# Kernel tuning notes

Measured on AMD Instinct MI355X. Metric: run time of the kernel, lower is better.

The kernel has to match this reference:

```python
import jax, jax.numpy as jnp
import numpy as np

IN, OUT, STEPS, BATCH = 1024, 1024, 100, 64
THR = 15.0
RATIO = 0.5
C1 = RATIO * THR            # initial membrane potential = 7.5
C2 = 1.0 / THR
C3 = (1.0 - RATIO) / STEPS


def setup_inputs() -> dict:
    key = jax.random.key(0)
    k0, k1, k2, k3 = jax.random.split(key, 4)
    spikes = jax.random.randint(k0, (STEPS, BATCH, IN), 0, 2).astype(jnp.float32)
    mem = jnp.full((BATCH, OUT), C1, dtype=jnp.float32)          # init_if
    hat_spikes = jax.random.uniform(k1, (BATCH, IN), dtype=jnp.float32)
    W = jax.random.normal(k2, (OUT, IN), dtype=jnp.float32)      # w_mean=0, w_std=1
    b = jax.random.normal(k3, (OUT,), dtype=jnp.float32)
    return {"spikes": spikes, "mem": mem, "hat_spikes": hat_spikes, "W": W, "b": b}


def reference(spikes, mem, hat_spikes, W, b):
    steps = spikes.shape[0]
    # delta_us = fc(spikes): [T, B, OUT]
    delta_us = jnp.einsum('tbi,oi->tbo', spikes, W) + b

    def step(carry, du):
        m, su = carry
        m = m + du
        s = (m > THR).astype(m.dtype)          # spike
        m = jnp.clip(m, 0.0, THR)              # clamp_(0, thr)
        su = su + m                            # sum_u += mem
        m = m - m * s                          # reset fired neurons
        return (m, su), s

    (mem_out, sum_u), ss = jax.lax.scan(
        step, (mem, jnp.zeros_like(mem)), delta_us)

    hat_u_fwd = sum_u / steps                  # [B, OUT]
    hat_s_fwd = ss.mean(axis=0)                # [B, OUT]

    # training-mode surrogate path: forward values come from the spike loop,
    # gradients flow through fc(hat_spikes) (ForwardFirstBackwardSecond)
    delta_u = hat_spikes @ W.T + b
    hat_u = jax.lax.stop_gradient(hat_u_fwd) + delta_u - jax.lax.stop_gradient(delta_u)
    surr = jnp.maximum(hat_u * C2, C3)         # (hat_u*C2).clamp_min(C3)
    hat_s = jax.lax.stop_gradient(hat_s_fwd) + surr - jax.lax.stop_gradient(surr)

    return ss, mem_out, hat_s
```

## Files before the change

### kernel.cpp

```cpp
#include <hip/hip_runtime.h>


typedef __attribute__((ext_vector_type(4))) int int4v;

#define T_STEPS 100
#define T_PAD   112
#define BO      65536
#define K_DIM   1024
#define A8_OFF  0
#define BT_OFF  7340032

__global__ __launch_bounds__(256)
void prepass(const float* __restrict__ S, const float* __restrict__ W,
             signed char* __restrict__ A8, signed char* __restrict__ Bt) {
    const int wave = blockIdx.x * 4 + (threadIdx.x >> 6);
    const int lane = threadIdx.x & 63;
    const int r16 = lane & 15, quad = lane >> 4;

    if (wave < 7168) {
        const int b   = wave / 112;
        const int rem = wave - b * 112;
        const int jt  = rem >> 4, k64 = rem & 15;
        const int t   = jt * 16 + r16;
        union { signed char c[16]; int4v v; } u;
        if (t < T_STEPS) {
            const float* sp = S + ((size_t)t * 64 + b) * K_DIM + k64 * 64 + quad * 16;
            const float4 s0 = *(const float4*)(sp);
            const float4 s1 = *(const float4*)(sp + 4);
            const float4 s2 = *(const float4*)(sp + 8);
            const float4 s3 = *(const float4*)(sp + 12);
            const float sv[16] = {s0.x,s0.y,s0.z,s0.w, s1.x,s1.y,s1.z,s1.w,
                                  s2.x,s2.y,s2.z,s2.w, s3.x,s3.y,s3.z,s3.w};
#pragma unroll
            for (int e = 0; e < 16; ++e) u.c[e] = (signed char)sv[e];
        } else {
#pragma unroll
            for (int e = 0; e < 16; ++e) u.c[e] = 0;
        }
        *(int4v*)(A8 + (size_t)wave * 1024 + lane * 16) = u.v;
    } else {
        const int t2 = wave - 7168;
        const int n16 = t2 >> 4, k64 = t2 & 15;
        const int n = n16 * 16 + r16;
        const float* wp = W + (size_t)n * K_DIM + k64 * 64 + quad * 16;
        const float4 w0 = *(const float4*)(wp);
        const float4 w1 = *(const float4*)(wp + 4);
        const float4 w2 = *(const float4*)(wp + 8);
        const float4 w3 = *(const float4*)(wp + 12);
        const float wv[16] = {w0.x,w0.y,w0.z,w0.w, w1.x,w1.y,w1.z,w1.w,
                              w2.x,w2.y,w2.z,w2.w, w3.x,w3.y,w3.z,w3.w};
        union { signed char c[16]; int4v v; } u[4];
#pragma unroll
        for (int e = 0; e < 16; ++e) {
            long long q = llrint((double)wv[e] * 0x1p28);
#pragma unroll
            for (int p = 0; p < 3; ++p) {
                const int d = (int)(((q + 128) & 255) - 128);
                u[p].c[e] = (signed char)d;
                q = (q - d) >> 8;
            }
            u[3].c[e] = (signed char)q;
        }
        signed char* base = Bt + (size_t)(n16 * 16 + k64) * 4 * 1024 + lane * 16;
#pragma unroll
        for (int p = 0; p < 4; ++p)
            *(int4v*)(base + (size_t)p * 1024) = u[p].v;
    }
}

__global__ __launch_bounds__(64, 2)
void gemm_scan(const signed char* __restrict__ A8,
               const signed char* __restrict__ Bt,
               const float* __restrict__ bias,
               const float* __restrict__ mem0,
               float* __restrict__ out) {
    __shared__ double dulds[T_STEPS * 16];

    const int bid = blockIdx.x;
    const int ng  = bid >> 6;
    const int b   = bid & 63;

    const int lane = threadIdx.x & 63;
    const int quad = lane >> 4, r16 = lane & 15;

    const signed char* abase = A8 + (size_t)b * T_PAD * 1024 + lane * 16;
    const signed char* bbase = Bt + (size_t)ng * 65536 + lane * 16;

    int4v acc[7][4] = {};

    for (int kt = 0; kt < 16; ++kt) {
        int4v af[7], bf[4];
#pragma unroll
        for (int i = 0; i < 7; ++i)
            af[i] = *(const int4v*)(abase + (size_t)(i * 16 + kt) * 1024);
#pragma unroll
        for (int p = 0; p < 4; ++p)
            bf[p] = *(const int4v*)(bbase + (size_t)(kt * 4 + p) * 1024);
#pragma unroll
        for (int p = 0; p < 4; ++p)
#pragma unroll
            for (int i = 0; i < 7; ++i)
                acc[i][p] = __builtin_amdgcn_mfma_i32_16x16x64_i8(
                    af[i], bf[p], acc[i][p], 0, 0, 0);
    }

    const double bd = (double)bias[ng * 16 + r16];
#pragma unroll
    for (int i = 0; i < 7; ++i)
#pragma unroll
        for (int e = 0; e < 4; ++e) {
            const int t = i * 16 + quad * 4 + e;
            if (t < T_STEPS) {
                long long v = (long long)acc[i][3][e];
                v = v * 256 + (long long)acc[i][2][e];
                v = v * 256 + (long long)acc[i][1][e];
                v = v * 256 + (long long)acc[i][0][e];
                dulds[t * 16 + r16] = (double)v * 0x1p-28 + bd;
            }
        }
    __syncthreads();

    if (lane < 16) {
        const int bo = b * 1024 + ng * 16 + lane;
        double m = (double)mem0[bo];
        double cnt = 0.0;
        double d[4];
#pragma unroll
        for (int u = 0; u < 4; ++u) d[u] = dulds[u * 16 + lane];
        for (int g = 0; g < 25; ++g) {
            double dn[4];
            if (g + 1 < 25) {
#pragma unroll
                for (int u = 0; u < 4; ++u) dn[u] = dulds[((g + 1) * 4 + u) * 16 + lane];
            }
#pragma unroll
            for (int u = 0; u < 4; ++u) {
                m += d[u];
                const double s = (m > 15.0) ? 1.0 : 0.0;
                m = fmin(fmax(m, 0.0), 15.0);
                out[(size_t)(g * 4 + u) * BO + bo] = (float)s;
                cnt += s;
                m -= m * s;
            }
            if (g + 1 < 25) {
#pragma unroll
                for (int u = 0; u < 4; ++u) d[u] = dn[u];
            }
        }
        out[(size_t)T_STEPS * BO + bo] = (float)m;
        out[(size_t)(T_STEPS + 1) * BO + bo] = (float)(cnt * 0.01);
    }
}

extern "C" void kernel_launch(void* const* d_in, const int* in_sizes, int n_in,
                              void* d_out, int out_size, void* d_ws, size_t ws_size,
                              hipStream_t stream) {
    const float* spikes = (const float*)d_in[0];
    const float* mem    = (const float*)d_in[1];
    const float* W      = (const float*)d_in[3];
    const float* b      = (const float*)d_in[4];
    float* out = (float*)d_out;
    signed char* A8 = (signed char*)d_ws + A8_OFF;
    signed char* Bt = (signed char*)d_ws + BT_OFF;

    prepass<<<dim3(2048), 256, 0, stream>>>(spikes, W, A8, Bt);
    gemm_scan<<<dim3(4096), 64, 0, stream>>>(A8, Bt, b, mem, out);
}
```

Measured before the change: 122.7 us.

## Process two neuron groups per block, overlapping first group's scan with second GEMM

```diff
diff --git a/kernel.cpp b/kernel.cpp
--- a/kernel.cpp
+++ b/kernel.cpp
@@ -68,6 +68,66 @@
     }
 }
 
+
+#define GEMM_LOAD(BB, KT)                                                     \
+    {                                                                         \
+        _Pragma("unroll")                                                     \
+        for (int i = 0; i < 7; ++i)                                           \
+            af[i] = *(const int4v*)(abase + (size_t)(i * 16 + (KT)) * 1024);  \
+        _Pragma("unroll")                                                     \
+        for (int p = 0; p < 4; ++p)                                           \
+            bf[p] = *(const int4v*)((BB) + (size_t)((KT) * 4 + p) * 1024);    \
+    }
+
+#define GEMM_MFMA()                                                           \
+    {                                                                         \
+        __builtin_amdgcn_s_setprio(1);                                        \
+        _Pragma("unroll")                                                     \
+        for (int p = 0; p < 4; ++p)                                           \
+            _Pragma("unroll")                                                 \
+            for (int i = 0; i < 7; ++i)                                       \
+                acc[i][p] = __builtin_amdgcn_mfma_i32_16x16x64_i8(            \
+                    af[i], bf[p], acc[i][p], 0, 0, 0);                        \
+        __builtin_amdgcn_s_setprio(0);                                        \
+    }
+
+#define HORNER(NG)                                                            \
+    {                                                                         \
+        const double bd = (double)bias[(NG) * 16 + r16];                      \
+        _Pragma("unroll")                                                     \
+        for (int i = 0; i < 7; ++i)                                           \
+            _Pragma("unroll")                                                 \
+            for (int e = 0; e < 4; ++e) {                                     \
+                const int t = i * 16 + quad * 4 + e;                          \
+                if (t < T_STEPS) {                                            \
+                    long long v = (long long)acc[i][3][e];                    \
+                    v = v * 256 + (long long)acc[i][2][e];                    \
+                    v = v * 256 + (long long)acc[i][1][e];                    \
+                    v = v * 256 + (long long)acc[i][0][e];                    \
+                    dulds[t * 16 + r16] = (double)v * 0x1p-28 + bd;           \
+                }                                                             \
+            }                                                                 \
+    }
+
+#define SCAN_GROUP(M, CNT, BO_, G)                                            \
+    if (lane < 16) {                                                          \
+        _Pragma("unroll")                                                     \
+        for (int u = 0; u < 4; ++u) {                                         \
+            M += dulds[((G) * 4 + u) * 16 + lane];                            \
+            const double s_ = (M > 15.0) ? 1.0 : 0.0;                         \
+            M = fmin(fmax(M, 0.0), 15.0);                                     \
+            out[(size_t)((G) * 4 + u) * BO + (BO_)] = (float)s_;              \
+            CNT += s_;                                                        \
+            M -= M * s_;                                                      \
+        }                                                                     \
+    }
+
+#define SCAN_TAIL(M, CNT, BO_)                                                \
+    if (lane < 16) {                                                          \
+        out[(size_t)T_STEPS * BO + (BO_)] = (float)(M);                       \
+        out[(size_t)(T_STEPS + 1) * BO + (BO_)] = (float)((CNT) * 0.01);      \
+    }
+
 __global__ __launch_bounds__(64, 2)
 void gemm_scan(const signed char* __restrict__ A8,
                const signed char* __restrict__ Bt,
@@ -77,79 +137,59 @@
     __shared__ double dulds[T_STEPS * 16];
 
     const int bid = blockIdx.x;
-    const int ng  = bid >> 6;
+    const int ngA = bid >> 6;
     const int b   = bid & 63;
+    const int ngB = ngA + 32;
 
     const int lane = threadIdx.x & 63;
     const int quad = lane >> 4, r16 = lane & 15;
 
-    const signed char* abase = A8 + (size_t)b * T_PAD * 1024 + lane * 16;
-    const signed char* bbase = Bt + (size_t)ng * 65536 + lane * 16;
-
-    int4v acc[7][4] = {};
-
+    const signed char* abase  = A8 + (size_t)b * T_PAD * 1024 + lane * 16;
+    const signed char* bbaseA = Bt + (size_t)ngA * 65536 + lane * 16;
+    const signed char* bbaseB = Bt + (size_t)ngB * 65536 + lane * 16;
+
+    int4v acc[7][4];
+    int4v af[7], bf[4];
+
+#pragma unroll
+    for (int i = 0; i < 7; ++i)
+#pragma unroll
+        for (int p = 0; p < 4; ++p) acc[i][p] = (int4v){0, 0, 0, 0};
     for (int kt = 0; kt < 16; ++kt) {
-        int4v af[7], bf[4];
-#pragma unroll
-        for (int i = 0; i < 7; ++i)
-            af[i] = *(const int4v*)(abase + (size_t)(i * 16 + kt) * 1024);
-#pragma unroll
-        for (int p = 0; p < 4; ++p)
-            bf[p] = *(const int4v*)(bbase + (size_t)(kt * 4 + p) * 1024);
-#pragma unroll
-        for (int p = 0; p < 4; ++p)
-#pragma unroll
-            for (int i = 0; i < 7; ++i)
-                acc[i][p] = __builtin_amdgcn_mfma_i32_16x16x64_i8(
-                    af[i], bf[p], acc[i][p], 0, 0, 0);
-    }
-
-    const double bd = (double)bias[ng * 16 + r16];
+        GEMM_LOAD(bbaseA, kt);
+        GEMM_MFMA();
+    }
+    HORNER(ngA);
+    __syncthreads();
+
+    const int boA = b * 1024 + ngA * 16 + r16;
+    double mA = (double)mem0[boA];
+    double cntA = 0.0;
+
 #pragma unroll
     for (int i = 0; i < 7; ++i)
 #pragma unroll
-        for (int e = 0; e < 4; ++e) {
-            const int t = i * 16 + quad * 4 + e;
-            if (t < T_STEPS) {
-                long long v = (long long)acc[i][3][e];
-                v = v * 256 + (long long)acc[i][2][e];
-                v = v * 256 + (long long)acc[i][1][e];
-                v = v * 256 + (long long)acc[i][0][e];
-                dulds[t * 16 + r16] = (double)v * 0x1p-28 + bd;
-            }
-        }
+        for (int p = 0; p < 4; ++p) acc[i][p] = (int4v){0, 0, 0, 0};
+    for (int kt = 0; kt < 16; ++kt) {
+        GEMM_LOAD(bbaseB, kt);
+        SCAN_GROUP(mA, cntA, boA, kt);
+        GEMM_MFMA();
+    }
+    for (int g = 16; g < 25; ++g) {
+        SCAN_GROUP(mA, cntA, boA, g);
+    }
+    SCAN_TAIL(mA, cntA, boA);
     __syncthreads();
-
-    if (lane < 16) {
-        const int bo = b * 1024 + ng * 16 + lane;
-        double m = (double)mem0[bo];
-        double cnt = 0.0;
-        double d[4];
-#pragma unroll
-        for (int u = 0; u < 4; ++u) d[u] = dulds[u * 16 + lane];
-        for (int g = 0; g < 25; ++g) {
-            double dn[4];
-            if (g + 1 < 25) {
-#pragma unroll
-                for (int u = 0; u < 4; ++u) dn[u] = dulds[((g + 1) * 4 + u) * 16 + lane];
-            }
-#pragma unroll
-            for (int u = 0; u < 4; ++u) {
-                m += d[u];
-                const double s = (m > 15.0) ? 1.0 : 0.0;
-                m = fmin(fmax(m, 0.0), 15.0);
-                out[(size_t)(g * 4 + u) * BO + bo] = (float)s;
-                cnt += s;
-                m -= m * s;
-            }
-            if (g + 1 < 25) {
-#pragma unroll
-                for (int u = 0; u < 4; ++u) d[u] = dn[u];
-            }
-        }
-        out[(size_t)T_STEPS * BO + bo] = (float)m;
-        out[(size_t)(T_STEPS + 1) * BO + bo] = (float)(cnt * 0.01);
-    }
+    HORNER(ngB);
+    __syncthreads();
+
+    const int boB = b * 1024 + ngB * 16 + r16;
+    double mB = (double)mem0[boB];
+    double cntB = 0.0;
+    for (int g = 0; g < 25; ++g) {
+        SCAN_GROUP(mB, cntB, boB, g);
+    }
+    SCAN_TAIL(mB, cntB, boB);
 }
 
 extern "C" void kernel_launch(void* const* d_in, const int* in_sizes, int n_in,
@@ -164,5 +204,5 @@
     signed char* Bt = (signed char*)d_ws + BT_OFF;
 
     prepass<<<dim3(2048), 256, 0, stream>>>(spikes, W, A8, Bt);
-    gemm_scan<<<dim3(4096), 64, 0, stream>>>(A8, Bt, b, mem, out);
+    gemm_scan<<<dim3(2048), 64, 0, stream>>>(A8, Bt, b, mem, out);
 }
```

Measured after the change: 124.5 us. About the same (+1.5%).

## Share spike A-panel across four waves via double-buffered LDS in gemm_scan

Applied to the files above, without the earlier changes.

```diff
diff --git a/kernel.cpp b/kernel.cpp
--- a/kernel.cpp
+++ b/kernel.cpp
@@ -37,7 +37,7 @@
 #pragma unroll
             for (int e = 0; e < 16; ++e) u.c[e] = 0;
         }
-        *(int4v*)(A8 + (size_t)wave * 1024 + lane * 16) = u.v;
+        *(int4v*)(A8 + ((size_t)(b * 112 + k64 * 7 + jt)) * 1024 + lane * 16) = u.v;
     } else {
         const int t2 = wave - 7168;
         const int n16 = t2 >> 4, k64 = t2 & 15;
@@ -68,43 +68,77 @@
     }
 }
 
-__global__ __launch_bounds__(64, 2)
+__global__ __launch_bounds__(256, 2)
 void gemm_scan(const signed char* __restrict__ A8,
                const signed char* __restrict__ Bt,
                const float* __restrict__ bias,
                const float* __restrict__ mem0,
                float* __restrict__ out) {
-    __shared__ double dulds[T_STEPS * 16];
+    __shared__ __align__(16) signed char ldsA[2][7168];
+    __shared__ float    hilds[T_STEPS][66];
+    __shared__ _Float16 lolds[T_STEPS][66];
 
     const int bid = blockIdx.x;
-    const int ng  = bid >> 6;
+    const int ngg = bid >> 6;
     const int b   = bid & 63;
 
-    const int lane = threadIdx.x & 63;
+    const int tid  = threadIdx.x;
+    const int lane = tid & 63, wid = tid >> 6;
     const int quad = lane >> 4, r16 = lane & 15;
 
-    const signed char* abase = A8 + (size_t)b * T_PAD * 1024 + lane * 16;
-    const signed char* bbase = Bt + (size_t)ng * 65536 + lane * 16;
+    const signed char* apan  = A8 + (size_t)b * (T_PAD * 1024) + lane * 16;
+    const signed char* bbase = Bt + (size_t)(ngg * 4 + wid) * 65536 + lane * 16;
 
     int4v acc[7][4] = {};
+    int4v bc[4], bn[4], stg0, stg1;
+
+#define STG_LOAD(KT)                                                          \
+    {                                                                         \
+        stg0 = *(const int4v*)(apan + ((size_t)(KT) * 7 + wid) * 1024);       \
+        if (wid < 3)                                                          \
+            stg1 = *(const int4v*)(apan + ((size_t)(KT) * 7 + wid + 4) * 1024); \
+    }
+#define STG_WRITE(BUF)                                                        \
+    {                                                                         \
+        *(int4v*)(&ldsA[BUF][wid * 1024 + lane * 16]) = stg0;                 \
+        if (wid < 3)                                                          \
+            *(int4v*)(&ldsA[BUF][(wid + 4) * 1024 + lane * 16]) = stg1;       \
+    }
+
+    STG_LOAD(0);
+    STG_WRITE(0);
+#pragma unroll
+    for (int p = 0; p < 4; ++p) bc[p] = *(const int4v*)(bbase + (size_t)p * 1024);
+    __syncthreads();
 
     for (int kt = 0; kt < 16; ++kt) {
-        int4v af[7], bf[4];
+        const int cur = kt & 1, nxt = cur ^ 1;
+        if (kt + 1 < 16) {
+            STG_LOAD(kt + 1);
+#pragma unroll
+            for (int p = 0; p < 4; ++p)
+                bn[p] = *(const int4v*)(bbase + (size_t)((kt + 1) * 4 + p) * 1024);
+        }
+        int4v af[7];
 #pragma unroll
         for (int i = 0; i < 7; ++i)
-            af[i] = *(const int4v*)(abase + (size_t)(i * 16 + kt) * 1024);
-#pragma unroll
-        for (int p = 0; p < 4; ++p)
-            bf[p] = *(const int4v*)(bbase + (size_t)(kt * 4 + p) * 1024);
+            af[i] = *(const int4v*)(&ldsA[cur][i * 1024 + lane * 16]);
 #pragma unroll
         for (int p = 0; p < 4; ++p)
 #pragma unroll
             for (int i = 0; i < 7; ++i)
                 acc[i][p] = __builtin_amdgcn_mfma_i32_16x16x64_i8(
-                    af[i], bf[p], acc[i][p], 0, 0, 0);
-    }
-
-    const double bd = (double)bias[ng * 16 + r16];
+                    af[i], bc[p], acc[i][p], 0, 0, 0);
+        if (kt + 1 < 16) {
+            STG_WRITE(nxt);
+#pragma unroll
+            for (int p = 0; p < 4; ++p) bc[p] = bn[p];
+        }
+        __syncthreads();
+    }
+
+    const int cb = wid * 16 + r16;
+    const double bd = (double)bias[ngg * 64 + cb];
 #pragma unroll
     for (int i = 0; i < 7; ++i)
 #pragma unroll
@@ -115,23 +149,31 @@
                 v = v * 256 + (long long)acc[i][2][e];
                 v = v * 256 + (long long)acc[i][1][e];
                 v = v * 256 + (long long)acc[i][0][e];
-                dulds[t * 16 + r16] = (double)v * 0x1p-28 + bd;
+                const double du = (double)v * 0x1p-28 + bd;
+                const float hi = (float)du;
+                hilds[t][cb] = hi;
+                lolds[t][cb] = (_Float16)((float)(du - (double)hi) * 4096.0f);
             }
         }
     __syncthreads();
 
-    if (lane < 16) {
-        const int bo = b * 1024 + ng * 16 + lane;
+    if (wid == 0) {
+        const int bo = b * 1024 + ngg * 64 + lane;
         double m = (double)mem0[bo];
         double cnt = 0.0;
         double d[4];
 #pragma unroll
-        for (int u = 0; u < 4; ++u) d[u] = dulds[u * 16 + lane];
+        for (int u = 0; u < 4; ++u)
+            d[u] = (double)hilds[u][lane] + (double)(float)lolds[u][lane] * 0x1p-12;
         for (int g = 0; g < 25; ++g) {
             double dn[4];
             if (g + 1 < 25) {
 #pragma unroll
-                for (int u = 0; u < 4; ++u) dn[u] = dulds[((g + 1) * 4 + u) * 16 + lane];
+                for (int u = 0; u < 4; ++u) {
+                    const int tt = (g + 1) * 4 + u;
+                    dn[u] = (double)hilds[tt][lane]
+                          + (double)(float)lolds[tt][lane] * 0x1p-12;
+                }
             }
 #pragma unroll
             for (int u = 0; u < 4; ++u) {
@@ -164,5 +206,5 @@
     signed char* Bt = (signed char*)d_ws + BT_OFF;
 
     prepass<<<dim3(2048), 256, 0, stream>>>(spikes, W, A8, Bt);
-    gemm_scan<<<dim3(4096), 64, 0, stream>>>(A8, Bt, b, mem, out);
+    gemm_scan<<<dim3(1024), 256, 0, stream>>>(A8, Bt, b, mem, out);
 }
```

New measurement: 124.4 us. Within noise of the previous version (+1.4%).
